# Performance work log

Measured on AMD Instinct MI355X. Metric: run time of the kernel, lower is better.

Reference implementation:

```python
import jax, jax.numpy as jnp
import numpy as np

B, T, D = 2, 2048, 1024
H, G, K = 16, 4, 64          # num_heads, num_kv_heads, head_dim
R = H // G                   # GQA repeat factor
F = 4096                     # mlp_dim
EPS = 1e-6


def rms_norm(x, scale, eps=EPS):
    var = jnp.mean(x.astype(jnp.float32) ** 2, axis=-1, keepdims=True)
    normed = x * jax.lax.rsqrt(var + eps)
    return (scale * normed).astype(x.dtype)


def apply_rope(x_BTHK, sin_BTK, cos_BTK):
    half = x_BTHK.shape[-1] // 2
    x1, x2 = x_BTHK[..., :half], x_BTHK[..., half:]
    s = sin_BTK[:, :, None, :]
    c = cos_BTK[:, :, None, :]
    return jnp.concatenate([x1 * c - x2 * s, x2 * c + x1 * s], axis=-1).astype(x_BTHK.dtype)


def setup_inputs() -> dict:
    key = jax.random.key(0)
    ks = jax.random.split(key, 12)
    hidden_BTD = jax.random.normal(ks[0], (B, T, D), jnp.float32)
    # rope tables: realistic sin/cos of position*inv_freq
    inv_freq = 1.0 / (10000.0 ** (jnp.arange(K // 2, dtype=jnp.float32) / (K // 2)))
    ang = jnp.arange(T, dtype=jnp.float32)[:, None] * inv_freq[None, :]  # [T, K/2]
    sin_BTK = jnp.broadcast_to(jnp.sin(ang)[None], (B, T, K // 2))
    cos_BTK = jnp.broadcast_to(jnp.cos(ang)[None], (B, T, K // 2))
    mask = jnp.broadcast_to(jnp.tril(jnp.ones((T, T), bool))[None], (B, T, T))
    sc = 1.0 / np.sqrt(D)
    scf = 1.0 / np.sqrt(F)
    return {
        "hidden_BTD": hidden_BTD, "sin_BTK": sin_BTK, "cos_BTK": cos_BTK, "mask": mask,
        "ln1_scale": jnp.ones((D,), jnp.float32),
        "ln2_scale": jnp.ones((D,), jnp.float32),
        "qn_scale": jnp.ones((K,), jnp.float32),
        "kn_scale": jnp.ones((K,), jnp.float32),
        "q_w": jax.random.normal(ks[1], (D, H * K), jnp.float32) * sc,
        "k_w": jax.random.normal(ks[2], (D, G * K), jnp.float32) * sc,
        "v_w": jax.random.normal(ks[3], (D, G * K), jnp.float32) * sc,
        "o_w": jax.random.normal(ks[4], (H * K, D), jnp.float32) * sc,
        "gate_w": jax.random.normal(ks[5], (D, F), jnp.float32) * sc,
        "up_w": jax.random.normal(ks[6], (D, F), jnp.float32) * sc,
        "down_w": jax.random.normal(ks[7], (F, D), jnp.float32) * scf,
    }


def reference(hidden_BTD, sin_BTK, cos_BTK, mask, ln1_scale, ln2_scale,
              qn_scale, kn_scale, q_w, k_w, v_w, o_w, gate_w, up_w, down_w):
    x = rms_norm(hidden_BTD, ln1_scale)
    q = rms_norm((x @ q_w).reshape(B, T, H, K), qn_scale)
    k = rms_norm((x @ k_w).reshape(B, T, G, K), kn_scale)
    v = (x @ v_w).reshape(B, T, G, K)
    q = apply_rope(q, sin_BTK, cos_BTK)
    k = apply_rope(k, sin_BTK, cos_BTK)
    q_BTGRK = q.reshape(B, T, G, R, K)
    scale = K ** (-0.5)
    logits = jnp.einsum('BTGRK,BSGK->BTSGR', q_BTGRK, k) * scale
    neg = float(jnp.finfo(logits.dtype).min)
    logits = jnp.where(mask[:, :, :, None, None], logits, neg)
    weights = jax.nn.softmax(logits.astype(jnp.float32), axis=2).astype(logits.dtype)
    attn = jnp.einsum('BTSGR,BSGK->BTGRK', weights, v).reshape(B, T, H * K)
    hidden_BTD = hidden_BTD + attn @ o_w
    y = rms_norm(hidden_BTD, ln2_scale)
    ff = (jax.nn.silu(y @ gate_w) * (y @ up_w)) @ down_w
    return hidden_BTD + ff
```

## Files before the change

### kernel.cpp

```cpp
#include <hip/hip_runtime.h>
#include <hip/hip_bf16.h>

#define EPSF 1e-6f
constexpr int Bsz  = 2;
constexpr int Tseq = 2048;
constexpr int Dmod = 1024;
constexpr int Hh   = 16;
constexpr int Gg   = 4;
constexpr int Ff   = 4096;
constexpr int Mrows = Bsz * Tseq;

typedef __attribute__((ext_vector_type(8))) short bf16x8;
typedef __attribute__((ext_vector_type(4))) float f32x4;
typedef unsigned short u16;

__device__ inline u16 f2bf(float x) {
    union { float f; unsigned u; } v; v.f = x;
    unsigned r = v.u + 0x7fff + ((v.u >> 16) & 1);
    return (u16)(r >> 16);
}
__device__ inline float bf2f(u16 h) {
    union { unsigned u; float f; } v; v.u = ((unsigned)h) << 16; return v.f;
}

__device__ __forceinline__ void async_copy16(const u16* g, u16* l) {
    __builtin_amdgcn_global_load_lds(
        (const __attribute__((address_space(1))) void*)g,
        (__attribute__((address_space(3))) void*)l, 16, 0, 0);
}


__global__ __launch_bounds__(256) void wprep_all_kernel(
    const float* __restrict__ q_w, const float* __restrict__ k_w,
    const float* __restrict__ v_w, const float* __restrict__ o_w,
    const float* __restrict__ gate_w, const float* __restrict__ up_w,
    const float* __restrict__ down_w,
    u16* __restrict__ QKVT, u16* __restrict__ OTh, u16* __restrict__ OTl,
    u16* __restrict__ GTh, u16* __restrict__ UTh, u16* __restrict__ DTh)
{
    const int bx = blockIdx.x;
    const float* W; u16* Th; u16* Tl = nullptr;
    int N, Kd, ntile, ktile, drow;
    if (bx < 1024) {
        W = q_w; N = 1024; Kd = 1024; ntile = bx & 31; ktile = bx >> 5;
        Th = QKVT; drow = ntile * 32;
    } else if (bx < 1280) {
        const int i = bx - 1024;
        W = k_w; N = 256; Kd = 1024; ntile = i & 7; ktile = i >> 3;
        Th = QKVT; drow = 1024 + ntile * 32;
    } else if (bx < 1536) {
        const int i = bx - 1280;
        W = v_w; N = 256; Kd = 1024; ntile = i & 7; ktile = i >> 3;
        Th = QKVT; drow = 1280 + ntile * 32;
    } else if (bx < 2560) {
        const int i = bx - 1536;
        W = o_w; N = 1024; Kd = 1024; ntile = i & 31; ktile = i >> 5;
        Th = OTh; Tl = OTl; drow = ntile * 32;
    } else if (bx < 6656) {
        const int i = bx - 2560;
        W = gate_w; N = 4096; Kd = 1024; ntile = i & 127; ktile = i >> 7;
        Th = GTh; drow = ntile * 32;
    } else if (bx < 10752) {
        const int i = bx - 6656;
        W = up_w; N = 4096; Kd = 1024; ntile = i & 127; ktile = i >> 7;
        Th = UTh; drow = ntile * 32;
    } else {
        const int i = bx - 10752;
        W = down_w; N = 1024; Kd = 4096; ntile = i & 31; ktile = i >> 5;
        Th = DTh; drow = ntile * 32;
    }
    const int n0 = ntile * 32, k0 = ktile * 32;

    __shared__ float tile[32][33];
    const int r = threadIdx.x >> 3, c4 = (threadIdx.x & 7) * 4;
    const float4 v = *reinterpret_cast<const float4*>(&W[(size_t)(k0 + r) * N + n0 + c4]);
    tile[r][c4 + 0] = v.x; tile[r][c4 + 1] = v.y;
    tile[r][c4 + 2] = v.z; tile[r][c4 + 3] = v.w;
    __syncthreads();
    const int nl = threadIdx.x >> 3, kq = (threadIdx.x & 7) * 4;
    float x0 = tile[kq + 0][nl], x1 = tile[kq + 1][nl];
    float x2 = tile[kq + 2][nl], x3 = tile[kq + 3][nl];
    ushort4 h;
    h.x = f2bf(x0); h.y = f2bf(x1); h.z = f2bf(x2); h.w = f2bf(x3);
    *reinterpret_cast<ushort4*>(&Th[(size_t)(drow + nl) * Kd + k0 + kq]) = h;
    if (Tl) {
        ushort4 l;
        l.x = f2bf(x0 - bf2f(h.x)); l.y = f2bf(x1 - bf2f(h.y));
        l.z = f2bf(x2 - bf2f(h.z)); l.w = f2bf(x3 - bf2f(h.w));
        *reinterpret_cast<ushort4*>(&Tl[(size_t)(drow + nl) * Kd + k0 + kq]) = l;
    }
}

template <int LO>
__global__ __launch_bounds__(256) void rmsnorm_split_kernel(
    const float* __restrict__ x, const float* __restrict__ scale,
    u16* __restrict__ oh, u16* __restrict__ ol)
{
    const int row = blockIdx.x;
    const int tid = threadIdx.x;
    const float4 v = reinterpret_cast<const float4*>(x + (size_t)row * Dmod)[tid];
    float ss = v.x * v.x + v.y * v.y + v.z * v.z + v.w * v.w;
    #pragma unroll
    for (int off = 32; off; off >>= 1) ss += __shfl_xor(ss, off, 64);
    __shared__ float part[4];
    if ((tid & 63) == 0) part[tid >> 6] = ss;
    __syncthreads();
    const float tot = part[0] + part[1] + part[2] + part[3];
    const float rstd = rsqrtf(tot * (1.0f / Dmod) + EPSF);
    const float4 sc = reinterpret_cast<const float4*>(scale)[tid];
    float o0 = v.x * rstd * sc.x, o1 = v.y * rstd * sc.y;
    float o2 = v.z * rstd * sc.z, o3 = v.w * rstd * sc.w;
    ushort4 h;
    h.x = f2bf(o0); h.y = f2bf(o1); h.z = f2bf(o2); h.w = f2bf(o3);
    *reinterpret_cast<ushort4*>(&oh[(size_t)row * Dmod + tid * 4]) = h;
    if (LO) {
        ushort4 l;
        l.x = f2bf(o0 - bf2f(h.x)); l.y = f2bf(o1 - bf2f(h.y));
        l.z = f2bf(o2 - bf2f(h.z)); l.w = f2bf(o3 - bf2f(h.w));
        *reinterpret_cast<ushort4*>(&ol[(size_t)row * Dmod + tid * 4]) = l;
    }
}

template <int NKT, int ASPLIT, int BSPLIT, int RES>
__global__ __launch_bounds__(256, 2) void mfma_gemm_pipe(
    const u16* __restrict__ Ah, const u16* __restrict__ Al,
    const u16* __restrict__ Bh, const u16* __restrict__ Bl,
    const float* __restrict__ res, float* __restrict__ C,
    int M, int N)
{
    constexpr int Kd = NKT * 32;
    constexpr int NI = 4 + 4 * ASPLIT * 0 + 2 * ASPLIT + 2 * BSPLIT;
    static_assert((NKT - 2) % 3 == 0, "main loop unroll-3");

    __shared__ u16 AsH[3][128 * 32];
    __shared__ u16 BsH[3][128 * 32];
    __shared__ u16 AsL[ASPLIT ? 3 : 1][128 * 32];
    __shared__ u16 BsL[BSPLIT ? 3 : 1][128 * 32];

    const int tid = threadIdx.x;
    const int lane = tid & 63, wave = tid >> 6;
    const int wm = (wave >> 1) * 64, wn = (wave & 1) * 64;
    const int m0 = blockIdx.y * 128, n0 = blockIdx.x * 128;
    const int fm = lane & 15, quad = lane >> 4;
    const int fsw = (fm >> 1) & 3;
    const int fcol = (quad ^ fsw) * 8;

    f32x4 acc[4][4];
    #pragma unroll
    for (int i = 0; i < 4; ++i)
        #pragma unroll
        for (int j = 0; j < 4; ++j) acc[i][j] = (f32x4){0.f, 0.f, 0.f, 0.f};

    const int srow = tid >> 2;
    const int schk = tid & 3;
    const int sw   = schk ^ ((srow >> 1) & 3);
    const u16* aS0 = &Ah[(size_t)(m0 + srow) * Kd + sw * 8];
    const u16* aS1 = &Ah[(size_t)(m0 + srow + 64) * Kd + sw * 8];
    const u16* bS0 = &Bh[(size_t)(n0 + srow) * Kd + sw * 8];
    const u16* bS1 = &Bh[(size_t)(n0 + srow + 64) * Kd + sw * 8];
    const u16* alS0 = ASPLIT ? &Al[(size_t)(m0 + srow) * Kd + sw * 8] : nullptr;
    const u16* alS1 = ASPLIT ? &Al[(size_t)(m0 + srow + 64) * Kd + sw * 8] : nullptr;
    const u16* blS0 = BSPLIT ? &Bl[(size_t)(n0 + srow) * Kd + sw * 8] : nullptr;
    const u16* blS1 = BSPLIT ? &Bl[(size_t)(n0 + srow + 64) * Kd + sw * 8] : nullptr;
    const int dst0 = srow * 32 + schk * 8;
    const int dst1 = dst0 + 64 * 32;

#define PSTAGE(T, BUF) do {                                                  \
        async_copy16(aS0 + (T) * 32, &AsH[BUF][dst0]);                       \
        async_copy16(aS1 + (T) * 32, &AsH[BUF][dst1]);                       \
        if (ASPLIT) {                                                        \
            async_copy16(alS0 + (T) * 32, &AsL[BUF][dst0]);                  \
            async_copy16(alS1 + (T) * 32, &AsL[BUF][dst1]);                  \
        }                                                                    \
        async_copy16(bS0 + (T) * 32, &BsH[BUF][dst0]);                       \
        async_copy16(bS1 + (T) * 32, &BsH[BUF][dst1]);                       \
        if (BSPLIT) {                                                        \
            async_copy16(blS0 + (T) * 32, &BsL[BUF][dst0]);                  \
            async_copy16(blS1 + (T) * 32, &BsL[BUF][dst1]);                  \
        }                                                                    \
    } while (0)

#define PGATE(GATE) do {                                                     \
        if ((GATE) == 1) {                                                   \
            if constexpr (NI == 4)                                           \
                asm volatile("s_waitcnt vmcnt(4)" ::: "memory");             \
            else                                                             \
                asm volatile("s_waitcnt vmcnt(8)" ::: "memory");             \
        } else if ((GATE) == 0) {                                            \
            asm volatile("s_waitcnt vmcnt(0)" ::: "memory");                 \
        }                                                                    \
    } while (0)

#define PSTEP(BC, BN, T, PF, GATE) do {                                      \
    bf16x8 ah[4], bh[4], al[4], bl[4];                                       \
    _Pragma("unroll")                                                        \
    for (int t = 0; t < 4; ++t) {                                            \
        const int ra = (wm + t * 16 + fm) * 32 + fcol;                       \
        const int rb = (wn + t * 16 + fm) * 32 + fcol;                       \
        ah[t] = *reinterpret_cast<const bf16x8*>(&AsH[BC][ra]);              \
        bh[t] = *reinterpret_cast<const bf16x8*>(&BsH[BC][rb]);              \
        if (ASPLIT) al[t] = *reinterpret_cast<const bf16x8*>(&AsL[BC][ra]);  \
        if (BSPLIT) bl[t] = *reinterpret_cast<const bf16x8*>(&BsL[BC][rb]);  \
    }                                                                        \
    if (PF) PSTAGE((T) + 2, BN);                                             \
    __builtin_amdgcn_s_barrier();                                            \
    asm volatile("s_waitcnt lgkmcnt(0)" ::: "memory");                       \
    __builtin_amdgcn_sched_barrier(0);                                       \
    __builtin_amdgcn_s_setprio(1);                                           \
    _Pragma("unroll")                                                        \
    for (int mt = 0; mt < 4; ++mt)                                           \
        _Pragma("unroll")                                                    \
        for (int nt = 0; nt < 4; ++nt) {                                     \
            acc[mt][nt] = __builtin_amdgcn_mfma_f32_16x16x32_bf16(           \
                ah[mt], bh[nt], acc[mt][nt], 0, 0, 0);                       \
            if (BSPLIT)                                                      \
                acc[mt][nt] = __builtin_amdgcn_mfma_f32_16x16x32_bf16(       \
                    ah[mt], bl[nt], acc[mt][nt], 0, 0, 0);                   \
            if (ASPLIT)                                                      \
                acc[mt][nt] = __builtin_amdgcn_mfma_f32_16x16x32_bf16(       \
                    al[mt], bh[nt], acc[mt][nt], 0, 0, 0);                   \
        }                                                                    \
    __builtin_amdgcn_s_setprio(0);                                           \
    PGATE(GATE);                                                             \
    __builtin_amdgcn_s_barrier();                                            \
} while (0)

    PSTAGE(0, 0);
    PSTAGE(1, 1);
    PGATE(1);
    __builtin_amdgcn_s_barrier();

    #pragma unroll 1
    for (int t3 = 0; t3 < NKT - 2; t3 += 3) {
        PSTEP(0, 2, t3 + 0, true, 1);
        PSTEP(1, 0, t3 + 1, true, 1);
        PSTEP(2, 1, t3 + 2, true, 1);
    }
    PSTEP(0, 2, NKT - 2, false, 0);
    PSTEP(1, 0, NKT - 1, false, -1);

#undef PSTEP
#undef PGATE
#undef PSTAGE

    const int cr = (lane >> 4) * 4, cn = lane & 15;
    #pragma unroll
    for (int mt = 0; mt < 4; ++mt)
        #pragma unroll
        for (int nt = 0; nt < 4; ++nt)
            #pragma unroll
            for (int r = 0; r < 4; ++r) {
                const int gm = m0 + wm + mt * 16 + cr + r;
                const int gn = n0 + wn + nt * 16 + cn;
                float v = acc[mt][nt][r];
                if (RES) v += res[(size_t)gm * N + gn];
                C[(size_t)gm * N + gn] = v;
            }
}

__global__ __launch_bounds__(256, 2) void qkv_fused_kernel(
    const u16* __restrict__ Ah, const u16* __restrict__ Bh,
    const float* __restrict__ qn, const float* __restrict__ kn,
    const float* __restrict__ sinp, const float* __restrict__ cosp,
    u16* __restrict__ Qbh, u16* __restrict__ Qbl,
    u16* __restrict__ Kbh, u16* __restrict__ Kbl,
    u16* __restrict__ Vth, u16* __restrict__ Vtl)
{
    __shared__ u16 As_h[128 * 32];
    __shared__ u16 Bs_h[128 * 32];

    const int Kd = 1024;
    const int tid = threadIdx.x;
    const int lane = tid & 63, wave = tid >> 6;
    const int wm = (wave >> 1) * 64, wn = (wave & 1) * 64;
    const int m0 = blockIdx.y * 128, n0 = blockIdx.x * 128;
    const int fm = lane & 15, quad = lane >> 4;
    const int fsw = (fm >> 1) & 3;
    const int fcol = ((quad ^ fsw) * 8);

    f32x4 acc[4][4];
    #pragma unroll
    for (int i = 0; i < 4; ++i)
        #pragma unroll
        for (int j = 0; j < 4; ++j) acc[i][j] = (f32x4){0.f, 0.f, 0.f, 0.f};

    const int lrow = lane >> 2;
    const int lchunk = lane & 3;
    const int schunk = lchunk ^ ((lrow >> 1) & 3);

    for (int k0 = 0; k0 < Kd; k0 += 32) {
        __syncthreads();
        #pragma unroll
        for (int p = 0; p < 2; ++p) {
            const int row = wave * 32 + p * 16 + lrow;
            const size_t ga = (size_t)(m0 + row) * Kd + k0 + schunk * 8;
            const size_t gb = (size_t)(n0 + row) * Kd + k0 + schunk * 8;
            const int ls = row * 32 + lchunk * 8;
            async_copy16(&Ah[ga], &As_h[ls]);
            async_copy16(&Bh[gb], &Bs_h[ls]);
        }
        __syncthreads();

        bf16x8 ah[4], bh[4];
        #pragma unroll
        for (int t = 0; t < 4; ++t) {
            ah[t] = *reinterpret_cast<const bf16x8*>(&As_h[(wm + t * 16 + fm) * 32 + fcol]);
            bh[t] = *reinterpret_cast<const bf16x8*>(&Bs_h[(wn + t * 16 + fm) * 32 + fcol]);
        }
        #pragma unroll
        for (int mt = 0; mt < 4; ++mt)
            #pragma unroll
            for (int nt = 0; nt < 4; ++nt)
                acc[mt][nt] = __builtin_amdgcn_mfma_f32_16x16x32_bf16(
                    ah[mt], bh[nt], acc[mt][nt], 0, 0, 0);
    }

    const int gn0 = n0 + wn;
    const int l15 = lane & 15;

    if (gn0 < 1280) {
        const bool isQ = (gn0 < 1024);
        const float* nsc = isQ ? qn : kn;
        const float osc = isQ ? 0.125f : 1.0f;
        u16* __restrict__ oh = isQ ? Qbh : Kbh;
        u16* __restrict__ ol = isQ ? Qbl : Kbl;
        const int rowstride = isQ ? 1024 : 256;
        const int colbase = isQ ? gn0 : gn0 - 1024;
        float sc[4];
        #pragma unroll
        for (int nt = 0; nt < 4; ++nt) sc[nt] = nsc[nt * 16 + l15];

        #pragma unroll
        for (int mt = 0; mt < 4; ++mt)
            #pragma unroll
            for (int r = 0; r < 4; ++r) {
                const int bt = m0 + wm + mt * 16 + quad * 4 + r;
                float v[4];
                #pragma unroll
                for (int nt = 0; nt < 4; ++nt) v[nt] = acc[mt][nt][r];
                float ss = v[0] * v[0] + v[1] * v[1] + v[2] * v[2] + v[3] * v[3];
                #pragma unroll
                for (int off = 1; off < 16; off <<= 1)
                    ss += __shfl_xor(ss, off, 16);
                const float rstd = rsqrtf(ss * (1.0f / 64.0f) + EPSF);
                float nv[4];
                #pragma unroll
                for (int nt = 0; nt < 4; ++nt) nv[nt] = v[nt] * rstd * sc[nt];
                const float s0 = sinp[bt * 32 + l15];
                const float c0 = cosp[bt * 32 + l15];
                const float s1 = sinp[bt * 32 + 16 + l15];
                const float c1 = cosp[bt * 32 + 16 + l15];
                float o[4];
                o[0] = (nv[0] * c0 - nv[2] * s0) * osc;
                o[1] = (nv[1] * c1 - nv[3] * s1) * osc;
                o[2] = (nv[2] * c0 + nv[0] * s0) * osc;
                o[3] = (nv[3] * c1 + nv[1] * s1) * osc;
                #pragma unroll
                for (int nt = 0; nt < 4; ++nt) {
                    const size_t off = (size_t)bt * rowstride + colbase + nt * 16 + l15;
                    const u16 hi = f2bf(o[nt]);
                    oh[off] = hi;
                    ol[off] = f2bf(o[nt] - bf2f(hi));
                }
            }
    } else {
        const int g = (gn0 - 1280) >> 6;
        const int b = (m0 + wm) >> 11;
        const int tb = ((m0 + wm) & 2047) + quad * 4;
        #pragma unroll
        for (int mt = 0; mt < 4; ++mt)
            #pragma unroll
            for (int nt = 0; nt < 4; ++nt) {
                const float v0 = acc[mt][nt][0], v1 = acc[mt][nt][1];
                const float v2 = acc[mt][nt][2], v3 = acc[mt][nt][3];
                ushort4 hv, lv;
                hv.x = f2bf(v0); hv.y = f2bf(v1); hv.z = f2bf(v2); hv.w = f2bf(v3);
                lv.x = f2bf(v0 - bf2f(hv.x)); lv.y = f2bf(v1 - bf2f(hv.y));
                lv.z = f2bf(v2 - bf2f(hv.z)); lv.w = f2bf(v3 - bf2f(hv.w));
                const size_t off =
                    ((size_t)((b * 4 + g) * 64 + nt * 16 + l15)) * Tseq + tb + mt * 16;
                *reinterpret_cast<ushort4*>(&Vth[off]) = hv;
                *reinterpret_cast<ushort4*>(&Vtl[off]) = lv;
            }
    }
}

#define GU_PHASE_SYNC()                                       \
    __builtin_amdgcn_s_barrier();                             \
    asm volatile("s_waitcnt lgkmcnt(0)" ::: "memory");        \
    __builtin_amdgcn_sched_barrier(0)

#define GU_MFMA4(MBASE, AF)                                                      \
    _Pragma("unroll")                                                            \
    for (int mf = 0; mf < 4; ++mf) {                                             \
        accg[(MBASE) + mf][0] = __builtin_amdgcn_mfma_f32_16x16x32_bf16(         \
            AF[mf], bgf[0], accg[(MBASE) + mf][0], 0, 0, 0);                     \
        accu[(MBASE) + mf][0] = __builtin_amdgcn_mfma_f32_16x16x32_bf16(         \
            AF[mf], buf2[0], accu[(MBASE) + mf][0], 0, 0, 0);                    \
        accg[(MBASE) + mf][1] = __builtin_amdgcn_mfma_f32_16x16x32_bf16(         \
            AF[mf], bgf[1], accg[(MBASE) + mf][1], 0, 0, 0);                     \
        accu[(MBASE) + mf][1] = __builtin_amdgcn_mfma_f32_16x16x32_bf16(         \
            AF[mf], buf2[1], accu[(MBASE) + mf][1], 0, 0, 0);                    \
    }

__global__ __launch_bounds__(512, 2) void gateup8_kernel(
    const u16* __restrict__ Yh, const u16* __restrict__ Yl,
    const u16* __restrict__ Gw, const u16* __restrict__ Uw,
    u16* __restrict__ FF)
{
    constexpr int NK = 32;
    __shared__ u16 AsH[3][256 * 32];
    __shared__ u16 AsL[3][256 * 32];
    __shared__ u16 Gs[3][128 * 32];
    __shared__ u16 Us[3][128 * 32];

    const int tid  = threadIdx.x;
    const int lane = tid & 63;
    const int wave = tid >> 6;
    const int wave_m = wave >> 2;
    const int wave_n = wave & 3;

    const int wg  = blockIdx.x;
    const int xcd = wg & 7;
    const int idx = wg >> 3;
    const int ntile = xcd * 4 + (idx & 3);
    const int mtile = idx >> 2;
    const int m0 = mtile * 256, n0 = ntile * 128;

    const int fm = lane & 15, quad = lane >> 4;
    const int fsw = (fm >> 1) & 3;
    const int fcol = (quad ^ fsw) * 8;

    f32x4 accg[8][2], accu[8][2];
    #pragma unroll
    for (int i = 0; i < 8; ++i)
        #pragma unroll
        for (int j = 0; j < 2; ++j) {
            accg[i][j] = (f32x4){0.f, 0.f, 0.f, 0.f};
            accu[i][j] = (f32x4){0.f, 0.f, 0.f, 0.f};
        }

    const int srow = tid >> 2;
    const int schk = tid & 3;
    const int sw   = schk ^ ((srow >> 1) & 3);
    const u16* aSrc0 = &Yh[(size_t)(m0 + srow) * 1024 + sw * 8];
    const u16* aSrc1 = &Yh[(size_t)(m0 + srow + 128) * 1024 + sw * 8];
    const u16* lSrc0 = &Yl[(size_t)(m0 + srow) * 1024 + sw * 8];
    const u16* lSrc1 = &Yl[(size_t)(m0 + srow + 128) * 1024 + sw * 8];
    const u16* gSrc  = &Gw[(size_t)(n0 + srow) * 1024 + sw * 8];
    const u16* uSrc  = &Uw[(size_t)(n0 + srow) * 1024 + sw * 8];
    const int aDst0 = srow * 32 + schk * 8;
    const int aDst1 = aDst0 + 128 * 32;

#define STAGE_AH(T, BUF) do {                                  \
        async_copy16(aSrc0 + (T) * 32, &AsH[BUF][aDst0]);      \
        async_copy16(aSrc1 + (T) * 32, &AsH[BUF][aDst1]); } while (0)
#define STAGE_AL(T, BUF) do {                                  \
        async_copy16(lSrc0 + (T) * 32, &AsL[BUF][aDst0]);      \
        async_copy16(lSrc1 + (T) * 32, &AsL[BUF][aDst1]); } while (0)
#define STAGE_B(T, BUF) do {                                   \
        async_copy16(gSrc + (T) * 32, &Gs[BUF][aDst0]);        \
        async_copy16(uSrc + (T) * 32, &Us[BUF][aDst0]); } while (0)

    int raOff[8], rbOff[2];
    #pragma unroll
    for (int mf = 0; mf < 8; ++mf)
        raOff[mf] = (wave_m * 128 + mf * 16 + fm) * 32 + fcol;
    #pragma unroll
    for (int nf = 0; nf < 2; ++nf)
        rbOff[nf] = (wave_n * 32 + nf * 16 + fm) * 32 + fcol;

    STAGE_AH(0, 0); STAGE_AL(0, 0); STAGE_B(0, 0);
    STAGE_AH(1, 1); STAGE_AL(1, 1); STAGE_B(1, 1);
    asm volatile("s_waitcnt vmcnt(6)" ::: "memory");
    __builtin_amdgcn_s_barrier();

    int bcur = 0, bnxt = 2;
    #pragma unroll 1
    for (int t = 0; t < NK; ++t) {
        const bool pf = (t + 2 < NK);
        bf16x8 bgf[2], buf2[2];

        {
            #pragma unroll
            for (int nf = 0; nf < 2; ++nf) {
                bgf[nf]  = *reinterpret_cast<const bf16x8*>(&Gs[bcur][rbOff[nf]]);
                buf2[nf] = *reinterpret_cast<const bf16x8*>(&Us[bcur][rbOff[nf]]);
            }
            bf16x8 af[4];
            #pragma unroll
            for (int mf = 0; mf < 4; ++mf)
                af[mf] = *reinterpret_cast<const bf16x8*>(&AsH[bcur][raOff[mf]]);
            if (pf) STAGE_AH(t + 2, bnxt);
            GU_PHASE_SYNC();
            __builtin_amdgcn_s_setprio(1);
            GU_MFMA4(0, af);
            __builtin_amdgcn_s_setprio(0);
            __builtin_amdgcn_s_barrier();
        }
        {
            bf16x8 af[4];
            #pragma unroll
            for (int mf = 0; mf < 4; ++mf)
                af[mf] = *reinterpret_cast<const bf16x8*>(&AsH[bcur][raOff[mf + 4]]);
            if (pf) STAGE_AL(t + 2, bnxt);
            GU_PHASE_SYNC();
            __builtin_amdgcn_s_setprio(1);
            GU_MFMA4(4, af);
            __builtin_amdgcn_s_setprio(0);
            __builtin_amdgcn_s_barrier();
        }
        {
            bf16x8 af[4];
            #pragma unroll
            for (int mf = 0; mf < 4; ++mf)
                af[mf] = *reinterpret_cast<const bf16x8*>(&AsL[bcur][raOff[mf]]);
            if (pf) STAGE_B(t + 2, bnxt);
            GU_PHASE_SYNC();
            __builtin_amdgcn_s_setprio(1);
            GU_MFMA4(0, af);
            __builtin_amdgcn_s_setprio(0);
            __builtin_amdgcn_s_barrier();
        }
        {
            bf16x8 af[4];
            #pragma unroll
            for (int mf = 0; mf < 4; ++mf)
                af[mf] = *reinterpret_cast<const bf16x8*>(&AsL[bcur][raOff[mf + 4]]);
            GU_PHASE_SYNC();
            __builtin_amdgcn_s_setprio(1);
            GU_MFMA4(4, af);
            __builtin_amdgcn_s_setprio(0);
            if (t + 2 < NK) {
                asm volatile("s_waitcnt vmcnt(6)" ::: "memory");
            } else if (t + 1 < NK) {
                asm volatile("s_waitcnt vmcnt(0)" ::: "memory");
            }
            __builtin_amdgcn_s_barrier();
        }

        bcur = (bcur == 2) ? 0 : bcur + 1;
        bnxt = (bnxt == 2) ? 0 : bnxt + 1;
    }
#undef STAGE_AH
#undef STAGE_AL
#undef STAGE_B

    const int cr = quad * 4;
    #pragma unroll
    for (int mf = 0; mf < 8; ++mf)
        #pragma unroll
        for (int nf = 0; nf < 2; ++nf)
            #pragma unroll
            for (int r = 0; r < 4; ++r) {
                const int gm = m0 + wave_m * 128 + mf * 16 + cr + r;
                const int gn = n0 + wave_n * 32 + nf * 16 + fm;
                const float g = accg[mf][nf][r];
                const float ff = (g / (1.0f + __expf(-g))) * accu[mf][nf][r];
                FF[(size_t)gm * Ff + gn] = f2bf(ff);
            }
}

__global__ __launch_bounds__(256) void attn_mfma_kernel(
    const u16* __restrict__ Qh, const u16* __restrict__ Ql,
    const u16* __restrict__ Kh, const u16* __restrict__ Kl,
    const u16* __restrict__ Vth, const u16* __restrict__ Vtl,
    u16* __restrict__ AOh, u16* __restrict__ AOl)
{
    __shared__ u16 KsH[64 * 72];
    __shared__ u16 KsL[64 * 72];
    __shared__ u16 VsH[64 * 72];
    __shared__ u16 VsL[64 * 72];
    __shared__ u16 Ps[4][16 * 72];

    const int tid = threadIdx.x;
    const int wave = tid >> 6, lane = tid & 63;
    const int l15 = lane & 15, quad = lane >> 4;

    const int bg = blockIdx.x & 7;
    const int b = bg >> 2, g = bg & 3;
    const int win = 127 - (blockIdx.x >> 3);
    const int t0 = win * 16;
    const int h = g * 4 + wave;

    bf16x8 qh[2], ql[2];
    {
        const size_t qrow = (size_t)(b * Tseq + t0 + l15) * 1024 + h * 64;
        #pragma unroll
        for (int ks = 0; ks < 2; ++ks) {
            qh[ks] = *reinterpret_cast<const bf16x8*>(&Qh[qrow + ks * 32 + quad * 8]);
            ql[ks] = *reinterpret_cast<const bf16x8*>(&Ql[qrow + ks * 32 + quad * 8]);
        }
    }

    const int srow = tid >> 2;
    const int scol = (tid & 3) * 16;
    const size_t kgb = (size_t)(b * Tseq) * 256 + g * 64 + scol;
    const size_t vgb = (size_t)(bg * 64 + srow) * Tseq + scol;

    const int nit = t0 / 64 + 1;

    uint4 ck0, ck1, cl0, cl1, cv0, cv1, cw0, cw1;
    {
        const size_t ka = kgb + (size_t)srow * 256;
        ck0 = *reinterpret_cast<const uint4*>(&Kh[ka]);
        ck1 = *reinterpret_cast<const uint4*>(&Kh[ka + 8]);
        cl0 = *reinterpret_cast<const uint4*>(&Kl[ka]);
        cl1 = *reinterpret_cast<const uint4*>(&Kl[ka + 8]);
        cv0 = *reinterpret_cast<const uint4*>(&Vth[vgb]);
        cv1 = *reinterpret_cast<const uint4*>(&Vth[vgb + 8]);
        cw0 = *reinterpret_cast<const uint4*>(&Vtl[vgb]);
        cw1 = *reinterpret_cast<const uint4*>(&Vtl[vgb + 8]);
    }

    f32x4 oacc[4];
    #pragma unroll
    for (int nt = 0; nt < 4; ++nt) oacc[nt] = (f32x4){0.f, 0.f, 0.f, 0.f};
    float m_r[4], l_r[4];
    #pragma unroll
    for (int r = 0; r < 4; ++r) { m_r[r] = -1e30f; l_r[r] = 0.0f; }

    u16* psw = &Ps[wave][0];
    const int lb = srow * 72 + scol;

    for (int it = 0; it < nit; ++it) {
        const int s0 = it * 64;
        const bool diag = (it == nit - 1);

        __syncthreads();
        *reinterpret_cast<uint4*>(&KsH[lb])     = ck0;
        *reinterpret_cast<uint4*>(&KsH[lb + 8]) = ck1;
        *reinterpret_cast<uint4*>(&KsL[lb])     = cl0;
        *reinterpret_cast<uint4*>(&KsL[lb + 8]) = cl1;
        *reinterpret_cast<uint4*>(&VsH[lb])     = cv0;
        *reinterpret_cast<uint4*>(&VsH[lb + 8]) = cv1;
        *reinterpret_cast<uint4*>(&VsL[lb])     = cw0;
        *reinterpret_cast<uint4*>(&VsL[lb + 8]) = cw1;
        if (it + 1 < nit) {
            const size_t ka = kgb + (size_t)(s0 + 64 + srow) * 256;
            ck0 = *reinterpret_cast<const uint4*>(&Kh[ka]);
            ck1 = *reinterpret_cast<const uint4*>(&Kh[ka + 8]);
            cl0 = *reinterpret_cast<const uint4*>(&Kl[ka]);
            cl1 = *reinterpret_cast<const uint4*>(&Kl[ka + 8]);
            const size_t va = vgb + s0 + 64;
            cv0 = *reinterpret_cast<const uint4*>(&Vth[va]);
            cv1 = *reinterpret_cast<const uint4*>(&Vth[va + 8]);
            cw0 = *reinterpret_cast<const uint4*>(&Vtl[va]);
            cw1 = *reinterpret_cast<const uint4*>(&Vtl[va + 8]);
        }
        __syncthreads();

        f32x4 sacc[4];
        #pragma unroll
        for (int nt = 0; nt < 4; ++nt) sacc[nt] = (f32x4){0.f, 0.f, 0.f, 0.f};

        #pragma unroll
        for (int ks = 0; ks < 2; ++ks) {
            bf16x8 kfh[4], kfl[4];
            #pragma unroll
            for (int nt = 0; nt < 4; ++nt) {
                const int a = (nt * 16 + l15) * 72 + ks * 32 + quad * 8;
                kfh[nt] = *reinterpret_cast<const bf16x8*>(&KsH[a]);
                kfl[nt] = *reinterpret_cast<const bf16x8*>(&KsL[a]);
            }
            #pragma unroll
            for (int nt = 0; nt < 4; ++nt) {
                sacc[nt] = __builtin_amdgcn_mfma_f32_16x16x32_bf16(qh[ks], kfh[nt], sacc[nt], 0, 0, 0);
                sacc[nt] = __builtin_amdgcn_mfma_f32_16x16x32_bf16(ql[ks], kfh[nt], sacc[nt], 0, 0, 0);
                sacc[nt] = __builtin_amdgcn_mfma_f32_16x16x32_bf16(qh[ks], kfl[nt], sacc[nt], 0, 0, 0);
            }
        }

        if (diag) {
            #pragma unroll
            for (int nt = 0; nt < 4; ++nt) {
                const int sg = s0 + nt * 16 + l15;
                #pragma unroll
                for (int r = 0; r < 4; ++r)
                    if (sg > t0 + quad * 4 + r) sacc[nt][r] = -1e30f;
            }
        }

        #pragma unroll
        for (int r = 0; r < 4; ++r) {
            float mx = fmaxf(fmaxf(sacc[0][r], sacc[1][r]),
                             fmaxf(sacc[2][r], sacc[3][r]));
            #pragma unroll
            for (int off = 1; off < 16; off <<= 1)
                mx = fmaxf(mx, __shfl_xor(mx, off, 16));
            const float mnew = fmaxf(m_r[r], mx);
            const float alpha = __expf(m_r[r] - mnew);
            m_r[r] = mnew;

            float rs = 0.0f;
            #pragma unroll
            for (int nt = 0; nt < 4; ++nt) {
                const float p = __expf(sacc[nt][r] - mnew);
                sacc[nt][r] = p;
                rs += p;
            }
            #pragma unroll
            for (int off = 1; off < 16; off <<= 1)
                rs += __shfl_xor(rs, off, 16);
            l_r[r] = l_r[r] * alpha + rs;
            #pragma unroll
            for (int nt = 0; nt < 4; ++nt) oacc[nt][r] *= alpha;
            #pragma unroll
            for (int nt = 0; nt < 4; ++nt)
                psw[(quad * 4 + r) * 72 + nt * 16 + l15] = f2bf(sacc[nt][r]);
        }

        #pragma unroll
        for (int ks = 0; ks < 2; ++ks) {
            const bf16x8 pa = *reinterpret_cast<const bf16x8*>(
                &psw[l15 * 72 + ks * 32 + quad * 8]);
            bf16x8 vfh[4], vfl[4];
            #pragma unroll
            for (int nt = 0; nt < 4; ++nt) {
                const int a = (nt * 16 + l15) * 72 + ks * 32 + quad * 8;
                vfh[nt] = *reinterpret_cast<const bf16x8*>(&VsH[a]);
                vfl[nt] = *reinterpret_cast<const bf16x8*>(&VsL[a]);
            }
            #pragma unroll
            for (int nt = 0; nt < 4; ++nt) {
                oacc[nt] = __builtin_amdgcn_mfma_f32_16x16x32_bf16(pa, vfh[nt], oacc[nt], 0, 0, 0);
                oacc[nt] = __builtin_amdgcn_mfma_f32_16x16x32_bf16(pa, vfl[nt], oacc[nt], 0, 0, 0);
            }
        }
    }

    #pragma unroll
    for (int r = 0; r < 4; ++r) {
        const float inv = 1.0f / l_r[r];
        const size_t orow = (size_t)(b * Tseq + t0 + quad * 4 + r) * 1024 + h * 64;
        #pragma unroll
        for (int nt = 0; nt < 4; ++nt) {
            const float o = oacc[nt][r] * inv;
            const u16 hi = f2bf(o);
            AOh[orow + nt * 16 + l15] = hi;
            AOl[orow + nt * 16 + l15] = f2bf(o - bf2f(hi));
        }
    }
}

extern "C" void kernel_launch(void* const* d_in, const int* in_sizes, int n_in,
                              void* d_out, int out_size, void* d_ws,
                              size_t ws_size, hipStream_t stream)
{
    const float* hidden = (const float*)d_in[0];
    const float* sinp   = (const float*)d_in[1];
    const float* cosp   = (const float*)d_in[2];
    const float* ln1    = (const float*)d_in[4];
    const float* ln2    = (const float*)d_in[5];
    const float* qn     = (const float*)d_in[6];
    const float* kn     = (const float*)d_in[7];
    const float* q_w    = (const float*)d_in[8];
    const float* k_w    = (const float*)d_in[9];
    const float* v_w    = (const float*)d_in[10];
    const float* o_w    = (const float*)d_in[11];
    const float* gate_w = (const float*)d_in[12];
    const float* up_w   = (const float*)d_in[13];
    const float* down_w = (const float*)d_in[14];
    float* out = (float*)d_out;

    char* base = (char*)d_ws;
    u16*   OTh  = (u16*)(base);
    u16*   OTl  = (u16*)(base + 2097152);
    u16*   GTh  = (u16*)(base + 4194304);
    u16*   UTh  = (u16*)(base + 12582912);
    u16*   DTh  = (u16*)(base + 20971520);
    u16*   QKVT = (u16*)(base + 29360128);
    u16*   Xh   = (u16*)(base + 32505856);
    u16*   Qbh  = (u16*)(base + 40894464);
    u16*   Qbl  = (u16*)(base + 49283072);
    u16*   Kbh  = (u16*)(base + 57671680);
    u16*   Kbl  = (u16*)(base + 59768832);
    u16*   Vth  = (u16*)(base + 61865984);
    u16*   Vtl  = (u16*)(base + 63963136);
    u16*   AOh  = (u16*)(base + 66060288);
    u16*   AOl  = (u16*)(base + 74448896);
    u16*   FFh  = (u16*)(base + 82837504);

    float* H2 = (float*)Qbh;
    u16*   Yh = Kbh;
    u16*   Yl = AOh;

    wprep_all_kernel<<<14848, 256, 0, stream>>>(
        q_w, k_w, v_w, o_w, gate_w, up_w, down_w,
        QKVT, OTh, OTl, GTh, UTh, DTh);

    rmsnorm_split_kernel<0><<<Mrows, 256, 0, stream>>>(hidden, ln1, Xh, nullptr);

    qkv_fused_kernel<<<dim3(12, 32), 256, 0, stream>>>(
        Xh, QKVT, qn, kn, sinp, cosp, Qbh, Qbl, Kbh, Kbl, Vth, Vtl);

    attn_mfma_kernel<<<Bsz * Gg * (Tseq / 16), 256, 0, stream>>>(
        Qbh, Qbl, Kbh, Kbl, Vth, Vtl, AOh, AOl);

    mfma_gemm_pipe<32, 1, 1, 1><<<dim3(8, 32), 256, 0, stream>>>(
        AOh, AOl, OTh, OTl, hidden, H2, Mrows, Dmod);

    rmsnorm_split_kernel<1><<<Mrows, 256, 0, stream>>>(H2, ln2, Yh, Yl);

    gateup8_kernel<<<512, 512, 0, stream>>>(Yh, Yl, GTh, UTh, FFh);

    mfma_gemm_pipe<128, 0, 0, 1><<<dim3(8, 32), 256, 0, stream>>>(
        FFh, nullptr, DTh, nullptr, H2, out, Mrows, Dmod);
}
```

Baseline: 498.9 us.

## Pipeline QKV GEMM with triple-buffered async loads; square gate/up wave tiles

The fused QKV projection kernel moves from a single-buffered load/sync/compute loop to a triple-buffered prefetch pipeline. Tiles are staged two steps ahead, and it uses explicit vmcnt waits, barriers and MFMA priority raising, like the other GEMMs. This hides global-load latency behind the matrix math. The gate/up kernel also changes its per-wave tile from 128x32 to 64x64, which cuts the LDS fragment reads per MFMA: A fragments are read once per K step and reused across two phases. The cost is more LDS (three buffers) and more live fragment registers, which may lower occupancy.

```diff
diff --git a/kernel.cpp b/kernel.cpp
--- a/kernel.cpp
+++ b/kernel.cpp
@@ -129,7 +129,7 @@
     int M, int N)
 {
     constexpr int Kd = NKT * 32;
-    constexpr int NI = 4 + 4 * ASPLIT * 0 + 2 * ASPLIT + 2 * BSPLIT;
+    constexpr int NI = 4 + 2 * ASPLIT + 2 * BSPLIT;
     static_assert((NKT - 2) % 3 == 0, "main loop unroll-3");
 
     __shared__ u16 AsH[3][128 * 32];
@@ -266,10 +266,11 @@
     u16* __restrict__ Kbh, u16* __restrict__ Kbl,
     u16* __restrict__ Vth, u16* __restrict__ Vtl)
 {
-    __shared__ u16 As_h[128 * 32];
-    __shared__ u16 Bs_h[128 * 32];
-
-    const int Kd = 1024;
+    constexpr int Kd = 1024;
+    constexpr int NKT = 32;
+    __shared__ u16 As[3][128 * 32];
+    __shared__ u16 Bs[3][128 * 32];
+
     const int tid = threadIdx.x;
     const int lane = tid & 63, wave = tid >> 6;
     const int wm = (wave >> 1) * 64, wn = (wave & 1) * 64;
@@ -284,36 +285,68 @@
         #pragma unroll
         for (int j = 0; j < 4; ++j) acc[i][j] = (f32x4){0.f, 0.f, 0.f, 0.f};
 
-    const int lrow = lane >> 2;
-    const int lchunk = lane & 3;
-    const int schunk = lchunk ^ ((lrow >> 1) & 3);
-
-    for (int k0 = 0; k0 < Kd; k0 += 32) {
-        __syncthreads();
-        #pragma unroll
-        for (int p = 0; p < 2; ++p) {
-            const int row = wave * 32 + p * 16 + lrow;
-            const size_t ga = (size_t)(m0 + row) * Kd + k0 + schunk * 8;
-            const size_t gb = (size_t)(n0 + row) * Kd + k0 + schunk * 8;
-            const int ls = row * 32 + lchunk * 8;
-            async_copy16(&Ah[ga], &As_h[ls]);
-            async_copy16(&Bh[gb], &Bs_h[ls]);
-        }
-        __syncthreads();
-
-        bf16x8 ah[4], bh[4];
-        #pragma unroll
-        for (int t = 0; t < 4; ++t) {
-            ah[t] = *reinterpret_cast<const bf16x8*>(&As_h[(wm + t * 16 + fm) * 32 + fcol]);
-            bh[t] = *reinterpret_cast<const bf16x8*>(&Bs_h[(wn + t * 16 + fm) * 32 + fcol]);
-        }
-        #pragma unroll
-        for (int mt = 0; mt < 4; ++mt)
-            #pragma unroll
-            for (int nt = 0; nt < 4; ++nt)
-                acc[mt][nt] = __builtin_amdgcn_mfma_f32_16x16x32_bf16(
-                    ah[mt], bh[nt], acc[mt][nt], 0, 0, 0);
-    }
+    const int srow = tid >> 2;
+    const int schk = tid & 3;
+    const int sw   = schk ^ ((srow >> 1) & 3);
+    const u16* aS0 = &Ah[(size_t)(m0 + srow) * Kd + sw * 8];
+    const u16* aS1 = &Ah[(size_t)(m0 + srow + 64) * Kd + sw * 8];
+    const u16* bS0 = &Bh[(size_t)(n0 + srow) * Kd + sw * 8];
+    const u16* bS1 = &Bh[(size_t)(n0 + srow + 64) * Kd + sw * 8];
+    const int dst0 = srow * 32 + schk * 8;
+    const int dst1 = dst0 + 64 * 32;
+
+#define QSTAGE(T, BUF) do {                                                  \
+        async_copy16(aS0 + (T) * 32, &As[BUF][dst0]);                        \
+        async_copy16(aS1 + (T) * 32, &As[BUF][dst1]);                        \
+        async_copy16(bS0 + (T) * 32, &Bs[BUF][dst0]);                        \
+        async_copy16(bS1 + (T) * 32, &Bs[BUF][dst1]);                        \
+    } while (0)
+
+#define QSTEP(BC, BN, T, PF, GATE) do {                                      \
+    bf16x8 ah[4], bh[4];                                                     \
+    _Pragma("unroll")                                                        \
+    for (int t = 0; t < 4; ++t) {                                            \
+        ah[t] = *reinterpret_cast<const bf16x8*>(                            \
+            &As[BC][(wm + t * 16 + fm) * 32 + fcol]);                        \
+        bh[t] = *reinterpret_cast<const bf16x8*>(                            \
+            &Bs[BC][(wn + t * 16 + fm) * 32 + fcol]);                        \
+    }                                                                        \
+    if (PF) QSTAGE((T) + 2, BN);                                             \
+    __builtin_amdgcn_s_barrier();                                            \
+    asm volatile("s_waitcnt lgkmcnt(0)" ::: "memory");                       \
+    __builtin_amdgcn_sched_barrier(0);                                       \
+    __builtin_amdgcn_s_setprio(1);                                           \
+    _Pragma("unroll")                                                        \
+    for (int mt = 0; mt < 4; ++mt)                                           \
+        _Pragma("unroll")                                                    \
+        for (int nt = 0; nt < 4; ++nt)                                       \
+            acc[mt][nt] = __builtin_amdgcn_mfma_f32_16x16x32_bf16(           \
+                ah[mt], bh[nt], acc[mt][nt], 0, 0, 0);                       \
+    __builtin_amdgcn_s_setprio(0);                                           \
+    if ((GATE) == 1) {                                                       \
+        asm volatile("s_waitcnt vmcnt(4)" ::: "memory");                     \
+    } else if ((GATE) == 0) {                                                \
+        asm volatile("s_waitcnt vmcnt(0)" ::: "memory");                     \
+    }                                                                        \
+    __builtin_amdgcn_s_barrier();                                            \
+} while (0)
+
+    QSTAGE(0, 0);
+    QSTAGE(1, 1);
+    asm volatile("s_waitcnt vmcnt(4)" ::: "memory");
+    __builtin_amdgcn_s_barrier();
+
+    #pragma unroll 1
+    for (int t3 = 0; t3 < NKT - 2; t3 += 3) {
+        QSTEP(0, 2, t3 + 0, true, 1);
+        QSTEP(1, 0, t3 + 1, true, 1);
+        QSTEP(2, 1, t3 + 2, true, 1);
+    }
+    QSTEP(0, 2, NKT - 2, false, 0);
+    QSTEP(1, 0, NKT - 1, false, -1);
+
+#undef QSTEP
+#undef QSTAGE
 
     const int gn0 = n0 + wn;
     const int l15 = lane & 15;
@@ -390,17 +423,17 @@
     asm volatile("s_waitcnt lgkmcnt(0)" ::: "memory");        \
     __builtin_amdgcn_sched_barrier(0)
 
-#define GU_MFMA4(MBASE, AF)                                                      \
+#define GU_MFMA16(AF, NB0)                                                       \
     _Pragma("unroll")                                                            \
     for (int mf = 0; mf < 4; ++mf) {                                             \
-        accg[(MBASE) + mf][0] = __builtin_amdgcn_mfma_f32_16x16x32_bf16(         \
-            AF[mf], bgf[0], accg[(MBASE) + mf][0], 0, 0, 0);                     \
-        accu[(MBASE) + mf][0] = __builtin_amdgcn_mfma_f32_16x16x32_bf16(         \
-            AF[mf], buf2[0], accu[(MBASE) + mf][0], 0, 0, 0);                    \
-        accg[(MBASE) + mf][1] = __builtin_amdgcn_mfma_f32_16x16x32_bf16(         \
-            AF[mf], bgf[1], accg[(MBASE) + mf][1], 0, 0, 0);                     \
-        accu[(MBASE) + mf][1] = __builtin_amdgcn_mfma_f32_16x16x32_bf16(         \
-            AF[mf], buf2[1], accu[(MBASE) + mf][1], 0, 0, 0);                    \
+        accg[mf][(NB0)] = __builtin_amdgcn_mfma_f32_16x16x32_bf16(               \
+            AF[mf], bgf[(NB0)], accg[mf][(NB0)], 0, 0, 0);                       \
+        accu[mf][(NB0)] = __builtin_amdgcn_mfma_f32_16x16x32_bf16(               \
+            AF[mf], buf2[(NB0)], accu[mf][(NB0)], 0, 0, 0);                      \
+        accg[mf][(NB0) + 1] = __builtin_amdgcn_mfma_f32_16x16x32_bf16(           \
+            AF[mf], bgf[(NB0) + 1], accg[mf][(NB0) + 1], 0, 0, 0);               \
+        accu[mf][(NB0) + 1] = __builtin_amdgcn_mfma_f32_16x16x32_bf16(           \
+            AF[mf], buf2[(NB0) + 1], accu[mf][(NB0) + 1], 0, 0, 0);              \
     }
 
 __global__ __launch_bounds__(512, 2) void gateup8_kernel(
@@ -417,8 +450,8 @@
     const int tid  = threadIdx.x;
     const int lane = tid & 63;
     const int wave = tid >> 6;
-    const int wave_m = wave >> 2;
-    const int wave_n = wave & 3;
+    const int wave_m = wave >> 1;
+    const int wave_n = wave & 1;
 
     const int wg  = blockIdx.x;
     const int xcd = wg & 7;
@@ -431,11 +464,11 @@
     const int fsw = (fm >> 1) & 3;
     const int fcol = (quad ^ fsw) * 8;
 
-    f32x4 accg[8][2], accu[8][2];
-    #pragma unroll
-    for (int i = 0; i < 8; ++i)
-        #pragma unroll
-        for (int j = 0; j < 2; ++j) {
+    f32x4 accg[4][4], accu[4][4];
+    #pragma unroll
+    for (int i = 0; i < 4; ++i)
+        #pragma unroll
+        for (int j = 0; j < 4; ++j) {
             accg[i][j] = (f32x4){0.f, 0.f, 0.f, 0.f};
             accu[i][j] = (f32x4){0.f, 0.f, 0.f, 0.f};
         }
@@ -462,13 +495,13 @@
         async_copy16(gSrc + (T) * 32, &Gs[BUF][aDst0]);        \
         async_copy16(uSrc + (T) * 32, &Us[BUF][aDst0]); } while (0)
 
-    int raOff[8], rbOff[2];
-    #pragma unroll
-    for (int mf = 0; mf < 8; ++mf)
-        raOff[mf] = (wave_m * 128 + mf * 16 + fm) * 32 + fcol;
-    #pragma unroll
-    for (int nf = 0; nf < 2; ++nf)
-        rbOff[nf] = (wave_n * 32 + nf * 16 + fm) * 32 + fcol;
+    int raOff[4], rbOff[4];
+    #pragma unroll
+    for (int mf = 0; mf < 4; ++mf)
+        raOff[mf] = (wave_m * 64 + mf * 16 + fm) * 32 + fcol;
+    #pragma unroll
+    for (int nf = 0; nf < 4; ++nf)
+        rbOff[nf] = (wave_n * 64 + nf * 16 + fm) * 32 + fcol;
 
     STAGE_AH(0, 0); STAGE_AL(0, 0); STAGE_B(0, 0);
     STAGE_AH(1, 1); STAGE_AL(1, 1); STAGE_B(1, 1);
@@ -479,57 +512,49 @@
     #pragma unroll 1
     for (int t = 0; t < NK; ++t) {
         const bool pf = (t + 2 < NK);
-        bf16x8 bgf[2], buf2[2];
+        bf16x8 bgf[4], buf2[4];
+        bf16x8 ahf[4];
 
         {
             #pragma unroll
-            for (int nf = 0; nf < 2; ++nf) {
+            for (int nf = 0; nf < 4; ++nf) {
                 bgf[nf]  = *reinterpret_cast<const bf16x8*>(&Gs[bcur][rbOff[nf]]);
                 buf2[nf] = *reinterpret_cast<const bf16x8*>(&Us[bcur][rbOff[nf]]);
             }
-            bf16x8 af[4];
             #pragma unroll
             for (int mf = 0; mf < 4; ++mf)
-                af[mf] = *reinterpret_cast<const bf16x8*>(&AsH[bcur][raOff[mf]]);
+                ahf[mf] = *reinterpret_cast<const bf16x8*>(&AsH[bcur][raOff[mf]]);
             if (pf) STAGE_AH(t + 2, bnxt);
             GU_PHASE_SYNC();
             __builtin_amdgcn_s_setprio(1);
-            GU_MFMA4(0, af);
+            GU_MFMA16(ahf, 0);
             __builtin_amdgcn_s_setprio(0);
             __builtin_amdgcn_s_barrier();
         }
         {
-            bf16x8 af[4];
-            #pragma unroll
-            for (int mf = 0; mf < 4; ++mf)
-                af[mf] = *reinterpret_cast<const bf16x8*>(&AsH[bcur][raOff[mf + 4]]);
             if (pf) STAGE_AL(t + 2, bnxt);
             GU_PHASE_SYNC();
             __builtin_amdgcn_s_setprio(1);
-            GU_MFMA4(4, af);
+            GU_MFMA16(ahf, 2);
             __builtin_amdgcn_s_setprio(0);
             __builtin_amdgcn_s_barrier();
         }
+        bf16x8 alf[4];
         {
-            bf16x8 af[4];
             #pragma unroll
             for (int mf = 0; mf < 4; ++mf)
-                af[mf] = *reinterpret_cast<const bf16x8*>(&AsL[bcur][raOff[mf]]);
+                alf[mf] = *reinterpret_cast<const bf16x8*>(&AsL[bcur][raOff[mf]]);
             if (pf) STAGE_B(t + 2, bnxt);
             GU_PHASE_SYNC();
             __builtin_amdgcn_s_setprio(1);
-            GU_MFMA4(0, af);
+            GU_MFMA16(alf, 0);
             __builtin_amdgcn_s_setprio(0);
             __builtin_amdgcn_s_barrier();
         }
         {
-            bf16x8 af[4];
-            #pragma unroll
-            for (int mf = 0; mf < 4; ++mf)
-                af[mf] = *reinterpret_cast<const bf16x8*>(&AsL[bcur][raOff[mf + 4]]);
             GU_PHASE_SYNC();
             __builtin_amdgcn_s_setprio(1);
-            GU_MFMA4(4, af);
+            GU_MFMA16(alf, 2);
             __builtin_amdgcn_s_setprio(0);
             if (t + 2 < NK) {
                 asm volatile("s_waitcnt vmcnt(6)" ::: "memory");
@@ -548,13 +573,13 @@
 
     const int cr = quad * 4;
     #pragma unroll
-    for (int mf = 0; mf < 8; ++mf)
-        #pragma unroll
-        for (int nf = 0; nf < 2; ++nf)
+    for (int mf = 0; mf < 4; ++mf)
+        #pragma unroll
+        for (int nf = 0; nf < 4; ++nf)
             #pragma unroll
             for (int r = 0; r < 4; ++r) {
-                const int gm = m0 + wave_m * 128 + mf * 16 + cr + r;
-                const int gn = n0 + wave_n * 32 + nf * 16 + fm;
+                const int gm = m0 + wave_m * 64 + mf * 16 + cr + r;
+                const int gn = n0 + wave_n * 64 + nf * 16 + fm;
                 const float g = accg[mf][nf][r];
                 const float ff = (g / (1.0f + __expf(-g))) * accu[mf][nf][r];
                 FF[(size_t)gm * Ff + gn] = f2bf(ff);
```

Result: no change. 496.2 us (-0.5%).
